# Performance work log

Hardware: AMD Instinct MI355X
Metric: run time of the kernel (lower is better)

The kernel has to match this reference:

```python
import jax, jax.numpy as jnp
import numpy as np

T, D, H, HD = 4096, 1536, 12, 128  # tokens, hidden, heads, head_dim
NEG = -1e9


def rotate_half(x):
    x1, x2 = jnp.split(x, 2, axis=-1)
    return jnp.concatenate((-x2, x1), axis=-1)


def setup_inputs() -> dict:
    key = jax.random.key(0)
    k1, k2, k3, k4 = jax.random.split(key, 4)
    hidden_states = jax.random.normal(k1, (T, D), dtype=jnp.float32)
    cu_seqlens = (jnp.arange(5, dtype=jnp.int32) * (T // 4))  # [0,1024,2048,3072,4096]
    # rotary angles: positions within each segment times inverse frequencies
    pos = jnp.arange(T, dtype=jnp.float32) % (T // 4)
    inv_freq = 1.0 / (10000.0 ** (jnp.arange(0, HD // 2, dtype=jnp.float32) / (HD // 2)))
    rotary_pos_emb = pos[:, None] * inv_freq[None, :]  # (T, HD//2)
    w_qkv = jax.random.normal(k2, (3 * D, D), dtype=jnp.float32) * (D ** -0.5)
    w_proj = jax.random.normal(k3, (D, D), dtype=jnp.float32) * (D ** -0.5)
    return {"hidden_states": hidden_states, "cu_seqlens": cu_seqlens,
            "rotary_pos_emb": rotary_pos_emb, "w_qkv": w_qkv, "w_proj": w_proj}


def reference(hidden_states, cu_seqlens, rotary_pos_emb, w_qkv, w_proj):
    seq_len = hidden_states.shape[0]
    scaling = HD ** -0.5
    # fused QKV projection: (T, 3D) -> (3, T, H, HD)
    qkv = (hidden_states @ w_qkv.T).reshape(seq_len, 3, H, HD).transpose(1, 0, 2, 3)
    q, k, v = qkv[0], qkv[1], qkv[2]
    # RoPE (vision style): emb = cat(rpe, rpe) along last dim
    emb = jnp.concatenate((rotary_pos_emb, rotary_pos_emb), axis=-1)  # (T, HD)
    cos = jnp.cos(emb)[:, None, :]  # (T, 1, HD) broadcast over heads
    sin = jnp.sin(emb)[:, None, :]
    q = q * cos + rotate_half(q) * sin
    k = k * cos + rotate_half(k) * sin
    # block-diagonal mask from cu_seqlens (varlen packing)
    seg_id = jnp.searchsorted(cu_seqlens[1:], jnp.arange(seq_len), side="right")
    block_mask = seg_id[:, None] == seg_id[None, :]  # (T, T) bool
    # attention per head: (H, T, HD)
    qh = q.transpose(1, 0, 2)
    kh = k.transpose(1, 0, 2)
    vh = v.transpose(1, 0, 2)
    scores = jnp.einsum("htd,hsd->hts", qh, kh) * scaling
    scores = jnp.where(block_mask[None, :, :], scores, NEG)
    attn = jax.nn.softmax(scores, axis=-1)
    out = jnp.einsum("hts,hsd->htd", attn, vh)  # (H, T, HD)
    out = out.transpose(1, 0, 2).reshape(seq_len, D)
    return out @ w_proj.T


if __name__ == "__main__":
    o = reference(**setup_inputs())
    print(o.shape, o.dtype)
```

## Files before the change

kernel.cpp:

```cpp
#include <hip/hip_runtime.h>
#include <stdint.h>

#define TT 4096
#define DD 1536
#define NH 12
#define HD_ 128

typedef __bf16 bf16x8 __attribute__((ext_vector_type(8)));
typedef float  f32x4  __attribute__((ext_vector_type(4)));
typedef float  f32x16 __attribute__((ext_vector_type(16)));

__device__ __forceinline__ unsigned short f2b(float f) {
  union { float f; uint32_t u; } x; x.f = f;
  uint32_t r = x.u + 0x7fffu + ((x.u >> 16) & 1u);
  return (unsigned short)(r >> 16);
}
__device__ __forceinline__ float b2f(unsigned short b) {
  union { uint32_t u; float f; } x; x.u = ((uint32_t)b) << 16;
  return x.f;
}

__device__ __forceinline__ f32x16 mfma32(bf16x8 a, bf16x8 b, f32x16 c) {
  return __builtin_amdgcn_mfma_f32_32x32x16_bf16(a, b, c, 0, 0, 0);
}

__device__ __forceinline__ void async16(const void* g, void* l) {
  __builtin_amdgcn_global_load_lds((const __attribute__((address_space(1))) uint32_t*)g,
                                   (__attribute__((address_space(3))) uint32_t*)l,
                                   16, 0, 0);
}

__global__ void cast_bf16_kernel(const float* __restrict__ in,
                                 unsigned short* __restrict__ out, int n) {
  int i = (blockIdx.x * blockDim.x + threadIdx.x) * 4;
  if (i + 3 < n) {
    float4 v = *reinterpret_cast<const float4*>(in + i);
    ushort4 o;
    o.x = f2b(v.x); o.y = f2b(v.y); o.z = f2b(v.z); o.w = f2b(v.w);
    *reinterpret_cast<ushort4*>(out + i) = o;
  }
}

__global__ void trig_table_kernel(const float* __restrict__ rpe,
                                  float* __restrict__ cs, float* __restrict__ sn) {
  int i = blockIdx.x * blockDim.x + threadIdx.x;
  float e = rpe[i];
  float s, c;
  sincosf(e, &s, &c);
  cs[i] = c;
  sn[i] = s;
}

__global__ __launch_bounds__(256, 4) void gemm_qkv_kernel(
    const unsigned short* __restrict__ A, const unsigned short* __restrict__ B,
    unsigned short* __restrict__ Qp, unsigned short* __restrict__ Kp,
    unsigned short* __restrict__ Vt, const float* __restrict__ csT,
    const float* __restrict__ snT) {
  __shared__ char smem[32768];
  const int tid = threadIdx.x;
  const int lane = tid & 63;
  const int wave = tid >> 6;
  const int wm = wave >> 1, wn = wave & 1;
  const int lr = lane & 15, lh = lane >> 4;

  const int m0 = blockIdx.x * 128;
  const int n0 = blockIdx.y * 128;

  const unsigned short* Ag = A + (size_t)(m0 + (tid >> 2)) * DD + (tid & 3) * 8;
  const unsigned short* Bg = B + (size_t)(n0 + (tid >> 2)) * DD + (tid & 3) * 8;

#define STAGE_G(BUF, K0)                                            \
  {                                                                 \
    unsigned short* la = (unsigned short*)(smem + (BUF) * 16384);   \
    unsigned short* lb = la + 4096;                                 \
    async16(Ag + (K0), &la[tid * 8]);                               \
    async16(Ag + (K0) + (size_t)64 * DD, &la[2048 + tid * 8]);      \
    async16(Bg + (K0), &lb[tid * 8]);                               \
    async16(Bg + (K0) + (size_t)64 * DD, &lb[2048 + tid * 8]);      \
  }

  f32x4 acc[4][4] = {};
  STAGE_G(0, 0);
  __syncthreads();
  int cur = 0;
  for (int k0 = 0; k0 < DD; k0 += 32) {
    const int kn = (k0 + 32 < DD) ? (k0 + 32) : k0;
    STAGE_G(cur ^ 1, kn);
    const unsigned short* la = (const unsigned short*)(smem + cur * 16384);
    const unsigned short* lb = la + 4096;
    bf16x8 af[4], bfr[4];
#pragma unroll
    for (int i = 0; i < 4; i++) {
      af[i]  = *reinterpret_cast<const bf16x8*>(&la[(wm * 64 + i * 16 + lr) * 32 + lh * 8]);
      bfr[i] = *reinterpret_cast<const bf16x8*>(&lb[(i * 32 + wn * 16 + lr) * 32 + lh * 8]);
    }
#pragma unroll
    for (int i = 0; i < 4; i++)
#pragma unroll
      for (int j = 0; j < 4; j++)
        acc[i][j] = __builtin_amdgcn_mfma_f32_16x16x32_bf16(af[i], bfr[j], acc[i][j], 0, 0, 0);
    __syncthreads();
    cur ^= 1;
  }
#undef STAGE_G

  const int s  = n0 / DD;
  const int hh = (n0 - s * DD) >> 7;

  if (s == 2) {
#pragma unroll
    for (int i = 0; i < 4; i++)
#pragma unroll
      for (int j = 0; j < 4; j++) {
        const int dd = j * 32 + wn * 16 + lr;
        const int t0 = m0 + wm * 64 + i * 16 + lh * 4;
        ushort4 st;
        st.x = f2b(acc[i][j][0]); st.y = f2b(acc[i][j][1]);
        st.z = f2b(acc[i][j][2]); st.w = f2b(acc[i][j][3]);
        *reinterpret_cast<ushort4*>(&Vt[((size_t)(hh * HD_ + dd)) * TT + t0]) = st;
      }
  } else {
    unsigned short* dst = (s == 0) ? Qp : Kp;
    const float scale =
        (s == 0) ? (0.08838834764831845f * 1.4426950408889634f) : 1.0f;
#pragma unroll
    for (int i = 0; i < 4; i++) {
#pragma unroll
      for (int j = 0; j < 4; j++) {
        const int dd = j * 32 + wn * 16 + lr;
        const int d2 = dd & 63;
        const float sgn = (dd < 64) ? -1.f : 1.f;
#pragma unroll
        for (int r = 0; r < 4; r++) {
          const int t = m0 + wm * 64 + i * 16 + lh * 4 + r;
          const float own = acc[i][j][r];
          const float par = acc[i][j ^ 2][r];
          const float c   = csT[t * 64 + d2];
          const float sn_ = snT[t * 64 + d2];
          dst[((size_t)hh * TT + t) * HD_ + dd] =
              f2b((own * c + sgn * par * sn_) * scale);
        }
        __builtin_amdgcn_sched_barrier(0);
      }
    }
  }
}

__global__ __launch_bounds__(512) void attn_kernel(
    const unsigned short* __restrict__ Qp, const unsigned short* __restrict__ Kp,
    const unsigned short* __restrict__ Vt, const int* __restrict__ cu,
    unsigned short* __restrict__ AO) {
  __shared__ unsigned short lds[32768];
  const int bid = blockIdx.x;
  const int tid = threadIdx.x;
  const int wave = tid >> 6;
  const int lane = tid & 63;
  const int lq = lane & 31;
  const int hi = lane >> 5;
  const int swz = lq & 7;

  const int xcd  = bid & 7;
  const int idx  = bid >> 3;
  const int pair = xcd * 6 + (idx >> 2);
  const int qblk = idx & 3;
  const int h    = pair >> 2;
  const int seg  = pair & 3;
  const int kstart = cu[seg], kend = cu[seg + 1];
  const int q0 = kstart + (qblk * 8 + wave) * 32;

  const unsigned short* Kh = Kp + (size_t)h * TT * HD_;
  const unsigned short* Vh = Vt + (size_t)h * HD_ * TT;

  const int krow0 = tid >> 4, kc0 = tid & 15;
  const int vrow0 = tid >> 3, vc0 = tid & 7;

#define STAGE_TILE(BUF, KT)                                                    \
  {                                                                            \
    unsigned short* Lk = &lds[(BUF) * 16384];                                  \
    unsigned short* Lv = Lk + 8192;                                            \
    _Pragma("unroll")                                                          \
    for (int r = 0; r < 2; r++) {                                              \
      int row = krow0 + r * 32;                                                \
      int c = kc0 ^ (row & 7);                                                 \
      async16(Kh + (size_t)((KT) + row) * HD_ + c * 8, Lk + tid * 8 + r * 4096); \
    }                                                                          \
    _Pragma("unroll")                                                          \
    for (int r = 0; r < 2; r++) {                                              \
      int row = vrow0 + r * 64;                                                \
      int c = vc0 ^ (row & 7);                                                 \
      async16(Vh + (size_t)row * TT + (KT) + c * 8, Lv + tid * 8 + r * 4096);  \
    }                                                                          \
  }

  const unsigned short* Qg = Qp + ((size_t)h * TT + q0 + lq) * HD_ + hi * 8;
  bf16x8 qf[8];
#pragma unroll
  for (int s = 0; s < 8; s++)
    qf[s] = *reinterpret_cast<const bf16x8*>(Qg + s * 16);

  STAGE_TILE(0, kstart);
  __syncthreads();

  f32x16 o0 = {}, o1 = {}, o2 = {}, o3 = {};
  float lsum = 0.f;
  int cur = 0;

  for (int kt = kstart; kt < kend; kt += 64) {
    const int ktn = (kt + 64 < kend) ? (kt + 64) : kt;
    STAGE_TILE(cur ^ 1, ktn);

    const unsigned short* Kl = &lds[cur * 16384];
    const unsigned short* Vl = Kl + 8192;

    f32x16 sA = {}, sB = {};
#pragma unroll
    for (int s = 0; s < 8; s++) {
      bf16x8 kf = *reinterpret_cast<const bf16x8*>(
          Kl + lq * 128 + (((s << 1) | hi) ^ swz) * 8);
      sA = mfma32(kf, qf[s], sA);
    }
#pragma unroll
    for (int s = 0; s < 8; s++) {
      bf16x8 kf = *reinterpret_cast<const bf16x8*>(
          Kl + 4096 + lq * 128 + (((s << 1) | hi) ^ swz) * 8);
      sB = mfma32(kf, qf[s], sB);
    }

    bf16x8 pfrag[4];
    float acc0 = 0.f, acc1 = 0.f;
#pragma unroll
    for (int g = 0; g < 4; g++) {
      const f32x16 S = (g & 2) ? sB : sA;
      const int b = (g & 1) * 8;
      float e0 = __builtin_amdgcn_exp2f(S[b + 0]);
      float e1 = __builtin_amdgcn_exp2f(S[b + 1]);
      float e2 = __builtin_amdgcn_exp2f(S[b + 2]);
      float e3 = __builtin_amdgcn_exp2f(S[b + 3]);
      float e4 = __builtin_amdgcn_exp2f(S[b + 4]);
      float e5 = __builtin_amdgcn_exp2f(S[b + 5]);
      float e6 = __builtin_amdgcn_exp2f(S[b + 6]);
      float e7 = __builtin_amdgcn_exp2f(S[b + 7]);
      acc0 += (e0 + e1) + (e2 + e3);
      acc1 += (e4 + e5) + (e6 + e7);
      union PW { uint32_t u; __bf16 e[2]; } p0, p1, p2, p3;
      p0.e[0] = (__bf16)e0; p0.e[1] = (__bf16)e1;
      p1.e[0] = (__bf16)e2; p1.e[1] = (__bf16)e3;
      p2.e[0] = (__bf16)e4; p2.e[1] = (__bf16)e5;
      p3.e[0] = (__bf16)e6; p3.e[1] = (__bf16)e7;
      uint32_t W2 = (uint32_t)__shfl_xor((int)(hi ? p0.u : p2.u), 32);
      uint32_t W3 = (uint32_t)__shfl_xor((int)(hi ? p1.u : p3.u), 32);
      union F { uint32_t w[4]; bf16x8 v; } f;
      f.w[0] = hi ? W2 : p0.u;
      f.w[1] = hi ? W3 : p1.u;
      f.w[2] = hi ? p2.u : W2;
      f.w[3] = hi ? p3.u : W3;
      pfrag[g] = f.v;
    }
    float tsum = acc0 + acc1;
    lsum += tsum + __shfl_xor(tsum, 32);

#pragma unroll
    for (int g = 0; g < 4; g++) {
      const int co = (((g << 1) | hi) ^ swz) * 8;
      bf16x8 v0 = *reinterpret_cast<const bf16x8*>(Vl + (lq)       * 64 + co);
      bf16x8 v1 = *reinterpret_cast<const bf16x8*>(Vl + (32 + lq)  * 64 + co);
      bf16x8 v2 = *reinterpret_cast<const bf16x8*>(Vl + (64 + lq)  * 64 + co);
      bf16x8 v3 = *reinterpret_cast<const bf16x8*>(Vl + (96 + lq)  * 64 + co);
      o0 = mfma32(v0, pfrag[g], o0);
      o1 = mfma32(v1, pfrag[g], o1);
      o2 = mfma32(v2, pfrag[g], o2);
      o3 = mfma32(v3, pfrag[g], o3);
    }

    __syncthreads();
    cur ^= 1;
  }
#undef STAGE_TILE

  const float inv = 1.0f / lsum;
  unsigned short* Ab = AO + (size_t)(q0 + lq) * DD + h * HD_ + 4 * hi;
#pragma unroll
  for (int dblk = 0; dblk < 4; dblk++) {
    f32x16 o = (dblk == 0) ? o0 : (dblk == 1) ? o1 : (dblk == 2) ? o2 : o3;
#pragma unroll
    for (int rq = 0; rq < 4; rq++) {
      ushort4 st;
      st.x = f2b(o[rq * 4 + 0] * inv);
      st.y = f2b(o[rq * 4 + 1] * inv);
      st.z = f2b(o[rq * 4 + 2] * inv);
      st.w = f2b(o[rq * 4 + 3] * inv);
      *reinterpret_cast<ushort4*>(Ab + dblk * 32 + rq * 8) = st;
    }
  }
}

__global__ __launch_bounds__(256, 4) void gemm_out_kernel(
    const unsigned short* __restrict__ A, const unsigned short* __restrict__ B,
    float* __restrict__ C) {
  __shared__ char smem[32768];
  const int tid = threadIdx.x;
  const int lane = tid & 63;
  const int wave = tid >> 6;
  const int wm = wave >> 1, wn = wave & 1;
  const int lr = lane & 15, lh = lane >> 4;
  const int m0 = blockIdx.x * 128, n0 = blockIdx.y * 128;
  const unsigned short* Ag = A + (size_t)(m0 + (tid >> 2)) * DD + (tid & 3) * 8;
  const unsigned short* Bg = B + (size_t)(n0 + (tid >> 2)) * DD + (tid & 3) * 8;

#define STAGE_G(BUF, K0)                                            \
  {                                                                 \
    unsigned short* la = (unsigned short*)(smem + (BUF) * 16384);   \
    unsigned short* lb = la + 4096;                                 \
    async16(Ag + (K0), &la[tid * 8]);                               \
    async16(Ag + (K0) + (size_t)64 * DD, &la[2048 + tid * 8]);      \
    async16(Bg + (K0), &lb[tid * 8]);                               \
    async16(Bg + (K0) + (size_t)64 * DD, &lb[2048 + tid * 8]);      \
  }

  f32x4 acc[4][4] = {};
  STAGE_G(0, 0);
  __syncthreads();
  int cur = 0;
  for (int k0 = 0; k0 < DD; k0 += 32) {
    const int kn = (k0 + 32 < DD) ? (k0 + 32) : k0;
    STAGE_G(cur ^ 1, kn);
    const unsigned short* la = (const unsigned short*)(smem + cur * 16384);
    const unsigned short* lb = la + 4096;
    bf16x8 af[4], bfr[4];
#pragma unroll
    for (int i = 0; i < 4; i++) {
      af[i]  = *reinterpret_cast<const bf16x8*>(&la[(wm * 64 + i * 16 + lr) * 32 + lh * 8]);
      bfr[i] = *reinterpret_cast<const bf16x8*>(&lb[(wn * 64 + i * 16 + lr) * 32 + lh * 8]);
    }
#pragma unroll
    for (int i = 0; i < 4; i++)
#pragma unroll
      for (int j = 0; j < 4; j++)
        acc[i][j] = __builtin_amdgcn_mfma_f32_16x16x32_bf16(af[i], bfr[j], acc[i][j], 0, 0, 0);
    __syncthreads();
    cur ^= 1;
  }
#undef STAGE_G

#pragma unroll
  for (int i = 0; i < 4; i++)
#pragma unroll
    for (int j = 0; j < 4; j++) {
      int cn = n0 + wn * 64 + j * 16 + lr;
#pragma unroll
      for (int r = 0; r < 4; r++) {
        int t = m0 + wm * 64 + i * 16 + lh * 4 + r;
        C[(size_t)t * DD + cn] = acc[i][j][r];
      }
    }
}

extern "C" void kernel_launch(void* const* d_in, const int* in_sizes, int n_in,
                              void* d_out, int out_size, void* d_ws, size_t ws_size,
                              hipStream_t stream) {
  const float* hs    = (const float*)d_in[0];
  const int*   cu    = (const int*)d_in[1];
  const float* rpe   = (const float*)d_in[2];
  const float* wqkv  = (const float*)d_in[3];
  const float* wproj = (const float*)d_in[4];
  float* out = (float*)d_out;
  char* ws = (char*)d_ws;

  unsigned short* hb = (unsigned short*)(ws + 0);
  unsigned short* wq = (unsigned short*)(ws + 12582912);
  unsigned short* wp = (unsigned short*)(ws + 26738688);
  unsigned short* Qp = (unsigned short*)(ws + 31457280);
  unsigned short* Kp = (unsigned short*)(ws + 44040192);
  unsigned short* Vt = (unsigned short*)(ws + 56623104);

  float* csT = (float*)wp;
  float* snT = csT + TT * 64;

  trig_table_kernel<<<1024, 256, 0, stream>>>(rpe, csT, snT);
  cast_bf16_kernel<<<6144, 256, 0, stream>>>(hs, hb, TT * DD);
  cast_bf16_kernel<<<6912, 256, 0, stream>>>(wqkv, wq, 3 * DD * DD);

  gemm_qkv_kernel<<<dim3(32, 36), 256, 0, stream>>>(hb, wq, Qp, Kp, Vt, csT, snT);

  cast_bf16_kernel<<<2304, 256, 0, stream>>>(wproj, wp, DD * DD);

  attn_kernel<<<192, 512, 0, stream>>>(Qp, Kp, Vt, cu, hb );

  gemm_out_kernel<<<dim3(32, 12), 256, 0, stream>>>(hb , wp, out);
}
```

Measured before the change: 174.5 us.

## Switch projection GEMMs to 32x32x16 MFMA and fuse prep kernels

Both projection GEMMs move from 16x16x32 MFMA tiles (4x4 per wave) to 32x32x16 MFMA tiles (2x2 per wave, two k-steps). The epilogue indexing for RoPE, V transpose and the output store is remapped to the 32x32 accumulator layout. The two cast launches and the trig-table launch are merged into one aux kernel to save launch overhead. The larger MFMA shape needs fewer LDS fragment reads per FLOP, but the new LDS read pattern may cause bank conflicts.

Measured after the change: 203.8 us. 1.17x slower.

```diff
diff --git a/kernel.cpp b/kernel.cpp
--- a/kernel.cpp
+++ b/kernel.cpp
@@ -28,6 +28,32 @@
   __builtin_amdgcn_global_load_lds((const __attribute__((address_space(1))) uint32_t*)g,
                                    (__attribute__((address_space(3))) uint32_t*)l,
                                    16, 0, 0);
+}
+
+__global__ void aux_kernel(const float* __restrict__ hs,
+                           const float* __restrict__ wqkv,
+                           const float* __restrict__ rpe,
+                           unsigned short* __restrict__ hb,
+                           unsigned short* __restrict__ wq,
+                           float* __restrict__ cs, float* __restrict__ sn) {
+  const int b = blockIdx.x;
+  if (b < 13056) {
+    const float* in = (b < 6144) ? hs : wqkv;
+    unsigned short* out = (b < 6144) ? hb : wq;
+    const int base = (b < 6144) ? b : (b - 6144);
+    int i = (base * 256 + threadIdx.x) * 4;
+    float4 v = *reinterpret_cast<const float4*>(in + i);
+    ushort4 o;
+    o.x = f2b(v.x); o.y = f2b(v.y); o.z = f2b(v.z); o.w = f2b(v.w);
+    *reinterpret_cast<ushort4*>(out + i) = o;
+  } else {
+    int i = (b - 13056) * 256 + threadIdx.x;
+    float e = rpe[i];
+    float s, c;
+    sincosf(e, &s, &c);
+    cs[i] = c;
+    sn[i] = s;
+  }
 }
 
 __global__ void cast_bf16_kernel(const float* __restrict__ in,
@@ -39,16 +65,6 @@
     o.x = f2b(v.x); o.y = f2b(v.y); o.z = f2b(v.z); o.w = f2b(v.w);
     *reinterpret_cast<ushort4*>(out + i) = o;
   }
-}
-
-__global__ void trig_table_kernel(const float* __restrict__ rpe,
-                                  float* __restrict__ cs, float* __restrict__ sn) {
-  int i = blockIdx.x * blockDim.x + threadIdx.x;
-  float e = rpe[i];
-  float s, c;
-  sincosf(e, &s, &c);
-  cs[i] = c;
-  sn[i] = s;
 }
 
 __global__ __launch_bounds__(256, 4) void gemm_qkv_kernel(
@@ -61,7 +77,7 @@
   const int lane = tid & 63;
   const int wave = tid >> 6;
   const int wm = wave >> 1, wn = wave & 1;
-  const int lr = lane & 15, lh = lane >> 4;
+  const int lq = lane & 31, hi = lane >> 5;
 
   const int m0 = blockIdx.x * 128;
   const int n0 = blockIdx.y * 128;
@@ -79,7 +95,7 @@
     async16(Bg + (K0) + (size_t)64 * DD, &lb[2048 + tid * 8]);      \
   }
 
-  f32x4 acc[4][4] = {};
+  f32x16 acc[2][2] = {};
   STAGE_G(0, 0);
   __syncthreads();
   int cur = 0;
@@ -88,17 +104,26 @@
     STAGE_G(cur ^ 1, kn);
     const unsigned short* la = (const unsigned short*)(smem + cur * 16384);
     const unsigned short* lb = la + 4096;
-    bf16x8 af[4], bfr[4];
-#pragma unroll
-    for (int i = 0; i < 4; i++) {
-      af[i]  = *reinterpret_cast<const bf16x8*>(&la[(wm * 64 + i * 16 + lr) * 32 + lh * 8]);
-      bfr[i] = *reinterpret_cast<const bf16x8*>(&lb[(i * 32 + wn * 16 + lr) * 32 + lh * 8]);
-    }
-#pragma unroll
-    for (int i = 0; i < 4; i++)
-#pragma unroll
-      for (int j = 0; j < 4; j++)
-        acc[i][j] = __builtin_amdgcn_mfma_f32_16x16x32_bf16(af[i], bfr[j], acc[i][j], 0, 0, 0);
+    bf16x8 af[2][2], bfr[2][2];
+#pragma unroll
+    for (int i = 0; i < 2; i++)
+#pragma unroll
+      for (int kk = 0; kk < 2; kk++)
+        af[i][kk] = *reinterpret_cast<const bf16x8*>(
+            &la[(wm * 64 + i * 32 + lq) * 32 + kk * 16 + hi * 8]);
+#pragma unroll
+    for (int j = 0; j < 2; j++)
+#pragma unroll
+      for (int kk = 0; kk < 2; kk++)
+        bfr[j][kk] = *reinterpret_cast<const bf16x8*>(
+            &lb[(wn * 32 + j * 64 + lq) * 32 + kk * 16 + hi * 8]);
+#pragma unroll
+    for (int i = 0; i < 2; i++)
+#pragma unroll
+      for (int j = 0; j < 2; j++) {
+        acc[i][j] = mfma32(af[i][0], bfr[j][0], acc[i][j]);
+        acc[i][j] = mfma32(af[i][1], bfr[j][1], acc[i][j]);
+      }
     __syncthreads();
     cur ^= 1;
   }
@@ -109,37 +134,45 @@
 
   if (s == 2) {
 #pragma unroll
-    for (int i = 0; i < 4; i++)
-#pragma unroll
-      for (int j = 0; j < 4; j++) {
-        const int dd = j * 32 + wn * 16 + lr;
-        const int t0 = m0 + wm * 64 + i * 16 + lh * 4;
-        ushort4 st;
-        st.x = f2b(acc[i][j][0]); st.y = f2b(acc[i][j][1]);
-        st.z = f2b(acc[i][j][2]); st.w = f2b(acc[i][j][3]);
-        *reinterpret_cast<ushort4*>(&Vt[((size_t)(hh * HD_ + dd)) * TT + t0]) = st;
+    for (int i = 0; i < 2; i++)
+#pragma unroll
+      for (int j = 0; j < 2; j++) {
+        const int dd = wn * 32 + j * 64 + lq;
+#pragma unroll
+        for (int g = 0; g < 4; g++) {
+          const int t0 = m0 + wm * 64 + i * 32 + g * 8 + hi * 4;
+          ushort4 st;
+          st.x = f2b(acc[i][j][g * 4 + 0]);
+          st.y = f2b(acc[i][j][g * 4 + 1]);
+          st.z = f2b(acc[i][j][g * 4 + 2]);
+          st.w = f2b(acc[i][j][g * 4 + 3]);
+          *reinterpret_cast<ushort4*>(&Vt[((size_t)(hh * HD_ + dd)) * TT + t0]) = st;
+        }
       }
   } else {
     unsigned short* dst = (s == 0) ? Qp : Kp;
     const float scale =
         (s == 0) ? (0.08838834764831845f * 1.4426950408889634f) : 1.0f;
 #pragma unroll
-    for (int i = 0; i < 4; i++) {
-#pragma unroll
-      for (int j = 0; j < 4; j++) {
-        const int dd = j * 32 + wn * 16 + lr;
+    for (int i = 0; i < 2; i++) {
+#pragma unroll
+      for (int j = 0; j < 2; j++) {
+        const int dd = wn * 32 + j * 64 + lq;
         const int d2 = dd & 63;
-        const float sgn = (dd < 64) ? -1.f : 1.f;
-#pragma unroll
-        for (int r = 0; r < 4; r++) {
-          const int t = m0 + wm * 64 + i * 16 + lh * 4 + r;
-          const float own = acc[i][j][r];
-          const float par = acc[i][j ^ 2][r];
-          const float c   = csT[t * 64 + d2];
-          const float sn_ = snT[t * 64 + d2];
-          dst[((size_t)hh * TT + t) * HD_ + dd] =
-              f2b((own * c + sgn * par * sn_) * scale);
-        }
+        const float sgn = (j == 0) ? -1.f : 1.f;
+#pragma unroll
+        for (int g = 0; g < 4; g++)
+#pragma unroll
+          for (int r = 0; r < 4; r++) {
+            const int reg = g * 4 + r;
+            const int t = m0 + wm * 64 + i * 32 + r + g * 8 + hi * 4;
+            const float own = acc[i][j][reg];
+            const float par = acc[i][j ^ 1][reg];
+            const float c   = csT[t * 64 + d2];
+            const float sn_ = snT[t * 64 + d2];
+            dst[((size_t)hh * TT + t) * HD_ + dd] =
+                f2b((own * c + sgn * par * sn_) * scale);
+          }
         __builtin_amdgcn_sched_barrier(0);
       }
     }
@@ -302,7 +335,7 @@
   const int lane = tid & 63;
   const int wave = tid >> 6;
   const int wm = wave >> 1, wn = wave & 1;
-  const int lr = lane & 15, lh = lane >> 4;
+  const int lq = lane & 31, hi = lane >> 5;
   const int m0 = blockIdx.x * 128, n0 = blockIdx.y * 128;
   const unsigned short* Ag = A + (size_t)(m0 + (tid >> 2)) * DD + (tid & 3) * 8;
   const unsigned short* Bg = B + (size_t)(n0 + (tid >> 2)) * DD + (tid & 3) * 8;
@@ -317,7 +350,7 @@
     async16(Bg + (K0) + (size_t)64 * DD, &lb[2048 + tid * 8]);      \
   }
 
-  f32x4 acc[4][4] = {};
+  f32x16 acc[2][2] = {};
   STAGE_G(0, 0);
   __syncthreads();
   int cur = 0;
@@ -326,32 +359,43 @@
     STAGE_G(cur ^ 1, kn);
     const unsigned short* la = (const unsigned short*)(smem + cur * 16384);
     const unsigned short* lb = la + 4096;
-    bf16x8 af[4], bfr[4];
-#pragma unroll
-    for (int i = 0; i < 4; i++) {
-      af[i]  = *reinterpret_cast<const bf16x8*>(&la[(wm * 64 + i * 16 + lr) * 32 + lh * 8]);
-      bfr[i] = *reinterpret_cast<const bf16x8*>(&lb[(wn * 64 + i * 16 + lr) * 32 + lh * 8]);
-    }
-#pragma unroll
-    for (int i = 0; i < 4; i++)
-#pragma unroll
-      for (int j = 0; j < 4; j++)
-        acc[i][j] = __builtin_amdgcn_mfma_f32_16x16x32_bf16(af[i], bfr[j], acc[i][j], 0, 0, 0);
+    bf16x8 af[2][2], bfr[2][2];
+#pragma unroll
+    for (int i = 0; i < 2; i++)
+#pragma unroll
+      for (int kk = 0; kk < 2; kk++)
+        af[i][kk] = *reinterpret_cast<const bf16x8*>(
+            &la[(wm * 64 + i * 32 + lq) * 32 + kk * 16 + hi * 8]);
+#pragma unroll
+    for (int j = 0; j < 2; j++)
+#pragma unroll
+      for (int kk = 0; kk < 2; kk++)
+        bfr[j][kk] = *reinterpret_cast<const bf16x8*>(
+            &lb[(wn * 64 + j * 32 + lq) * 32 + kk * 16 + hi * 8]);
+#pragma unroll
+    for (int i = 0; i < 2; i++)
+#pragma unroll
+      for (int j = 0; j < 2; j++) {
+        acc[i][j] = mfma32(af[i][0], bfr[j][0], acc[i][j]);
+        acc[i][j] = mfma32(af[i][1], bfr[j][1], acc[i][j]);
+      }
     __syncthreads();
     cur ^= 1;
   }
 #undef STAGE_G
 
 #pragma unroll
-  for (int i = 0; i < 4; i++)
-#pragma unroll
-    for (int j = 0; j < 4; j++) {
-      int cn = n0 + wn * 64 + j * 16 + lr;
-#pragma unroll
-      for (int r = 0; r < 4; r++) {
-        int t = m0 + wm * 64 + i * 16 + lh * 4 + r;
-        C[(size_t)t * DD + cn] = acc[i][j][r];
-      }
+  for (int i = 0; i < 2; i++)
+#pragma unroll
+    for (int j = 0; j < 2; j++) {
+      const int cn = n0 + wn * 64 + j * 32 + lq;
+#pragma unroll
+      for (int g = 0; g < 4; g++)
+#pragma unroll
+        for (int r = 0; r < 4; r++) {
+          const int t = m0 + wm * 64 + i * 32 + r + g * 8 + hi * 4;
+          C[(size_t)t * DD + cn] = acc[i][j][g * 4 + r];
+        }
     }
 }
 
@@ -376,9 +420,7 @@
   float* csT = (float*)wp;
   float* snT = csT + TT * 64;
 
-  trig_table_kernel<<<1024, 256, 0, stream>>>(rpe, csT, snT);
-  cast_bf16_kernel<<<6144, 256, 0, stream>>>(hs, hb, TT * DD);
-  cast_bf16_kernel<<<6912, 256, 0, stream>>>(wqkv, wq, 3 * DD * DD);
+  aux_kernel<<<14080, 256, 0, stream>>>(hs, wqkv, rpe, hb, wq, csT, snT);
 
   gemm_qkv_kernel<<<dim3(32, 36), 256, 0, stream>>>(hb, wq, Qp, Kp, Vt, csT, snT);
 
```

## Swizzle GEMM LDS tiles with XOR and fuse prep kernels into one launch

Applied to the files above, without the earlier changes.

The QKV and output GEMM kernels now XOR-swizzle the 16-byte chunk index by row when staging tiles into LDS, and read fragments back with the matching swizzle. This is meant to cut LDS bank conflicts on the fragment reads, since those rows have a 64-byte stride. The separate trig-table kernel and the two cast kernels are also merged into one aux kernel launch, which removes launch overhead and lets those small jobs overlap. The swizzle has to agree exactly between the staging and read sides, or the results will be wrong.

Result: faster. 169.0 us (-3.2%).

```diff
diff --git a/kernel.cpp b/kernel.cpp
--- a/kernel.cpp
+++ b/kernel.cpp
@@ -28,6 +28,32 @@
   __builtin_amdgcn_global_load_lds((const __attribute__((address_space(1))) uint32_t*)g,
                                    (__attribute__((address_space(3))) uint32_t*)l,
                                    16, 0, 0);
+}
+
+__global__ void aux_kernel(const float* __restrict__ hs,
+                           const float* __restrict__ wqkv,
+                           const float* __restrict__ rpe,
+                           unsigned short* __restrict__ hb,
+                           unsigned short* __restrict__ wq,
+                           float* __restrict__ cs, float* __restrict__ sn) {
+  const int b = blockIdx.x;
+  if (b < 13056) {
+    const float* in = (b < 6144) ? hs : wqkv;
+    unsigned short* out = (b < 6144) ? hb : wq;
+    const int base = (b < 6144) ? b : (b - 6144);
+    int i = (base * 256 + threadIdx.x) * 4;
+    float4 v = *reinterpret_cast<const float4*>(in + i);
+    ushort4 o;
+    o.x = f2b(v.x); o.y = f2b(v.y); o.z = f2b(v.z); o.w = f2b(v.w);
+    *reinterpret_cast<ushort4*>(out + i) = o;
+  } else {
+    int i = (b - 13056) * 256 + threadIdx.x;
+    float e = rpe[i];
+    float s, c;
+    sincosf(e, &s, &c);
+    cs[i] = c;
+    sn[i] = s;
+  }
 }
 
 __global__ void cast_bf16_kernel(const float* __restrict__ in,
@@ -39,16 +65,6 @@
     o.x = f2b(v.x); o.y = f2b(v.y); o.z = f2b(v.z); o.w = f2b(v.w);
     *reinterpret_cast<ushort4*>(out + i) = o;
   }
-}
-
-__global__ void trig_table_kernel(const float* __restrict__ rpe,
-                                  float* __restrict__ cs, float* __restrict__ sn) {
-  int i = blockIdx.x * blockDim.x + threadIdx.x;
-  float e = rpe[i];
-  float s, c;
-  sincosf(e, &s, &c);
-  cs[i] = c;
-  sn[i] = s;
 }
 
 __global__ __launch_bounds__(256, 4) void gemm_qkv_kernel(
@@ -66,8 +82,10 @@
   const int m0 = blockIdx.x * 128;
   const int n0 = blockIdx.y * 128;
 
-  const unsigned short* Ag = A + (size_t)(m0 + (tid >> 2)) * DD + (tid & 3) * 8;
-  const unsigned short* Bg = B + (size_t)(n0 + (tid >> 2)) * DD + (tid & 3) * 8;
+  const int srow = tid >> 2;
+  const int schunk = (tid & 3) ^ (srow & 3);
+  const unsigned short* Ag = A + (size_t)(m0 + srow) * DD + schunk * 8;
+  const unsigned short* Bg = B + (size_t)(n0 + srow) * DD + schunk * 8;
 
 #define STAGE_G(BUF, K0)                                            \
   {                                                                 \
@@ -79,6 +97,7 @@
     async16(Bg + (K0) + (size_t)64 * DD, &lb[2048 + tid * 8]);      \
   }
 
+  const int csw = (lr & 3);
   f32x4 acc[4][4] = {};
   STAGE_G(0, 0);
   __syncthreads();
@@ -91,8 +110,10 @@
     bf16x8 af[4], bfr[4];
 #pragma unroll
     for (int i = 0; i < 4; i++) {
-      af[i]  = *reinterpret_cast<const bf16x8*>(&la[(wm * 64 + i * 16 + lr) * 32 + lh * 8]);
-      bfr[i] = *reinterpret_cast<const bf16x8*>(&lb[(i * 32 + wn * 16 + lr) * 32 + lh * 8]);
+      af[i]  = *reinterpret_cast<const bf16x8*>(
+          &la[(wm * 64 + i * 16 + lr) * 32 + (lh ^ csw) * 8]);
+      bfr[i] = *reinterpret_cast<const bf16x8*>(
+          &lb[(i * 32 + wn * 16 + lr) * 32 + (lh ^ csw) * 8]);
     }
 #pragma unroll
     for (int i = 0; i < 4; i++)
@@ -304,8 +325,11 @@
   const int wm = wave >> 1, wn = wave & 1;
   const int lr = lane & 15, lh = lane >> 4;
   const int m0 = blockIdx.x * 128, n0 = blockIdx.y * 128;
-  const unsigned short* Ag = A + (size_t)(m0 + (tid >> 2)) * DD + (tid & 3) * 8;
-  const unsigned short* Bg = B + (size_t)(n0 + (tid >> 2)) * DD + (tid & 3) * 8;
+
+  const int srow = tid >> 2;
+  const int schunk = (tid & 3) ^ (srow & 3);
+  const unsigned short* Ag = A + (size_t)(m0 + srow) * DD + schunk * 8;
+  const unsigned short* Bg = B + (size_t)(n0 + srow) * DD + schunk * 8;
 
 #define STAGE_G(BUF, K0)                                            \
   {                                                                 \
@@ -317,6 +341,7 @@
     async16(Bg + (K0) + (size_t)64 * DD, &lb[2048 + tid * 8]);      \
   }
 
+  const int csw = (lr & 3);
   f32x4 acc[4][4] = {};
   STAGE_G(0, 0);
   __syncthreads();
@@ -329,8 +354,10 @@
     bf16x8 af[4], bfr[4];
 #pragma unroll
     for (int i = 0; i < 4; i++) {
-      af[i]  = *reinterpret_cast<const bf16x8*>(&la[(wm * 64 + i * 16 + lr) * 32 + lh * 8]);
-      bfr[i] = *reinterpret_cast<const bf16x8*>(&lb[(wn * 64 + i * 16 + lr) * 32 + lh * 8]);
+      af[i]  = *reinterpret_cast<const bf16x8*>(
+          &la[(wm * 64 + i * 16 + lr) * 32 + (lh ^ csw) * 8]);
+      bfr[i] = *reinterpret_cast<const bf16x8*>(
+          &lb[(wn * 64 + i * 16 + lr) * 32 + (lh ^ csw) * 8]);
     }
 #pragma unroll
     for (int i = 0; i < 4; i++)
@@ -376,9 +403,7 @@
   float* csT = (float*)wp;
   float* snT = csT + TT * 64;
 
-  trig_table_kernel<<<1024, 256, 0, stream>>>(rpe, csT, snT);
-  cast_bf16_kernel<<<6144, 256, 0, stream>>>(hs, hb, TT * DD);
-  cast_bf16_kernel<<<6912, 256, 0, stream>>>(wqkv, wq, 3 * DD * DD);
+  aux_kernel<<<14080, 256, 0, stream>>>(hs, wqkv, rpe, hb, wq, csT, snT);
 
   gemm_qkv_kernel<<<dim3(32, 36), 256, 0, stream>>>(hb, wq, Qp, Kp, Vt, csT, snT);
 
```
